# Performance work log

Hardware: AMD Instinct MI355X
Metric: run time of the kernel (lower is better)

## Reference

```python
import jax, jax.numpy as jnp
import numpy as np

DIM = 2048
H = 16
HD = 128
S = 2640          # frame_seq_len(22*40=880) * num_frame_per_block(3)
CACHE = 5280      # 6 cached frames
MAXPOS = 8192
EPS = 1e-6


def rmsnorm(x, g, eps=EPS):
    return x * jax.lax.rsqrt(jnp.mean(x * x, axis=-1, keepdims=True) + eps) * g


def apply_rope_interleaved(x, cos, sin):
    # x: [s, H, HD]; cos/sin: [s, HD//2]; is_neox=False -> adjacent pairs
    x1 = x[..., 0::2]
    x2 = x[..., 1::2]
    c = cos[:, None, :]
    s_ = sin[:, None, :]
    o1 = x1 * c - x2 * s_
    o2 = x2 * c + x1 * s_
    return jnp.stack([o1, o2], axis=-1).reshape(x.shape)


def setup_inputs() -> dict:
    key = jax.random.key(0)
    ks = jax.random.split(key, 10)
    w_scale = DIM ** -0.5
    x = jax.random.normal(ks[0], (1, S, DIM), dtype=jnp.float32)
    # cos_sin_cache: [max_pos, HD] = [cos(HD//2) | sin(HD//2)], real rope values
    inv_freq = 1.0 / (10000.0 ** (np.arange(0, HD, 2, dtype=np.float32) / HD))
    t = np.arange(MAXPOS, dtype=np.float32)
    ang = np.outer(t, inv_freq)  # [MAXPOS, HD//2]
    freqs = jnp.asarray(np.concatenate([np.cos(ang), np.sin(ang)], axis=1), dtype=jnp.float32)
    k_cache = jax.random.normal(ks[1], (CACHE, H, HD), dtype=jnp.float32)
    v_cache = jax.random.normal(ks[2], (CACHE, H, HD), dtype=jnp.float32)
    Wq = jax.random.normal(ks[3], (DIM, DIM), dtype=jnp.float32) * w_scale
    Wk = jax.random.normal(ks[4], (DIM, DIM), dtype=jnp.float32) * w_scale
    Wv = jax.random.normal(ks[5], (DIM, DIM), dtype=jnp.float32) * w_scale
    Wo = jax.random.normal(ks[6], (DIM, DIM), dtype=jnp.float32) * w_scale
    bq = jnp.zeros((DIM,), jnp.float32)
    bk = jnp.zeros((DIM,), jnp.float32)
    bv = jnp.zeros((DIM,), jnp.float32)
    bo = jnp.zeros((DIM,), jnp.float32)
    gq = jnp.ones((DIM,), jnp.float32)
    gk = jnp.ones((DIM,), jnp.float32)
    return {"x": x, "freqs": freqs, "k_cache": k_cache, "v_cache": v_cache,
            "Wq": Wq, "bq": bq, "Wk": Wk, "bk": bk, "Wv": Wv, "bv": bv,
            "Wo": Wo, "bo": bo, "gq": gq, "gk": gk, "current_start": CACHE}


def reference(x, freqs, k_cache, v_cache, Wq, bq, Wk, bk, Wv, bv, Wo, bo, gq, gk, current_start):
    s = x.shape[1]
    xf = x[0]                                   # [s, DIM], B==1
    q = rmsnorm(xf @ Wq.T + bq, gq).reshape(s, H, HD)
    k = rmsnorm(xf @ Wk.T + bk, gk).reshape(s, H, HD)
    v = (xf @ Wv.T + bv).reshape(s, H, HD)
    # fused RoPE via cos_sin_cache lookup, interleaved (is_neox=False)
    positions = jnp.arange(s, dtype=jnp.int32) + current_start
    cs = freqs[positions]                       # [s, HD]
    cos, sin = cs[:, : HD // 2], cs[:, HD // 2:]
    rq = apply_rope_interleaved(q, cos, sin)
    rk = apply_rope_interleaved(k, cos, sin)
    # streaming attention: full access to cache, causal within incoming block
    k_all = jnp.concatenate([k_cache, rk], axis=0)  # [L, H, HD]
    v_all = jnp.concatenate([v_cache, v], axis=0)
    L = k_all.shape[0]
    scale = HD ** -0.5
    scores = jnp.einsum("qhd,khd->hqk", rq, k_all) * scale  # [H, s, L]
    kv_idx = jnp.arange(L)
    q_idx = jnp.arange(s)
    mask = (kv_idx[None, :] - (L - s)) <= q_idx[:, None]    # cache always visible
    scores = jnp.where(mask[None, :, :], scores, jnp.float32(-1e30))
    attn = jax.nn.softmax(scores, axis=-1)
    out = jnp.einsum("hqk,khd->qhd", attn, v_all).reshape(s, DIM)
    y = out @ Wo.T + bo
    return y[None]                              # [1, s, DIM]
```

## Files before the change

kernel.cpp:

```cpp
#include <hip/hip_runtime.h>

#define DIMN 2048
#define NH 16
#define HDIM 128

typedef __attribute__((ext_vector_type(4))) float f32x4;
typedef __attribute__((ext_vector_type(16))) float f32x16;
typedef __attribute__((ext_vector_type(8))) __bf16 bfx8;
typedef __attribute__((ext_vector_type(4))) __bf16 bf16x4;
typedef __attribute__((ext_vector_type(2))) __bf16 bf16x2;
typedef __attribute__((ext_vector_type(8))) unsigned short u16x8;

__device__ __forceinline__ unsigned short f2bf(float f){
  unsigned u = __builtin_bit_cast(unsigned, f);
  u += 0x7fffu + ((u >> 16) & 1u);
  return (unsigned short)(u >> 16);
}
__device__ __forceinline__ float bf2f(unsigned short h){
  unsigned u = (unsigned)h << 16;
  return __builtin_bit_cast(float, u);
}

__device__ __forceinline__ void gl_lds16(const void* g, void* l){
  __builtin_amdgcn_global_load_lds((const __attribute__((address_space(1))) void*)g,
                                   (__attribute__((address_space(3))) void*)l, 16, 0, 0);
}

__device__ __forceinline__ int xcd_swz(int bid, int nwg){
  const int q = nwg >> 3, r = nwg & 7;
  const int xcd = bid & 7, idx = bid >> 3;
  return (xcd < r ? xcd*(q+1) : r*(q+1) + (xcd-r)*q) + idx;
}

#define MFMA16(a,b,c) __builtin_amdgcn_mfma_f32_16x16x32_bf16((a),(b),(c),0,0,0)
#define MFMA32(a,b,c) __builtin_amdgcn_mfma_f32_32x32x16_bf16((a),(b),(c),0,0,0)

__global__ __launch_bounds__(256) void cast_bf16_kernel(const float* __restrict__ in,
                                                        unsigned short* __restrict__ out, int n8){
  int i = blockIdx.x*256 + threadIdx.x;
  if (i >= n8) return;
  const float4* p = (const float4*)(in + (size_t)i*8);
  float4 a = p[0], b = p[1];
  u16x8 o;
  o[0]=f2bf(a.x); o[1]=f2bf(a.y); o[2]=f2bf(a.z); o[3]=f2bf(a.w);
  o[4]=f2bf(b.x); o[5]=f2bf(b.y); o[6]=f2bf(b.z); o[7]=f2bf(b.w);
  *(u16x8*)(out + (size_t)i*8) = o;
}

__global__ __launch_bounds__(256) void kcache_kernel(const float* __restrict__ kc,
                                                     unsigned short* __restrict__ kb,
                                                     int R, int L_){
  const int gid = blockIdx.x*256 + threadIdx.x;
  if (gid >= R*256) return;
  const size_t idx = (size_t)gid * 8;
  const int k   = (int)(idx >> 11);
  const int rem = (int)(idx & 2047);
  const int hh  = rem >> 7, d = rem & 127;
  const float4* p = (const float4*)(kc + idx);
  float4 a = p[0], b = p[1];
  u16x8 o;
  o[0]=f2bf(a.x); o[1]=f2bf(a.y); o[2]=f2bf(a.z); o[3]=f2bf(a.w);
  o[4]=f2bf(b.x); o[5]=f2bf(b.y); o[6]=f2bf(b.z); o[7]=f2bf(b.w);
  *(u16x8*)(kb + (size_t)hh*L_*HDIM + (size_t)k*HDIM + d) = o;
}

__global__ __launch_bounds__(256) void vtrans_kernel(const float* __restrict__ src,
                                                     unsigned short* __restrict__ vt,
                                                     int R, int koff, int L_){
  __shared__ __align__(16) unsigned short tile[32][72];
  const int kb0 = blockIdx.x * 64, db0 = blockIdx.y * 32, hh = blockIdx.z;
  const int t = threadIdx.x;
  const int kk = t >> 2, dd = (t & 3) * 8;
  const int k = kb0 + kk;
  if (k < R){
    const float* p = src + (size_t)k*DIMN + hh*HDIM + db0 + dd;
    float4 a = ((const float4*)p)[0], b = ((const float4*)p)[1];
    tile[dd+0][kk] = f2bf(a.x); tile[dd+1][kk] = f2bf(a.y);
    tile[dd+2][kk] = f2bf(a.z); tile[dd+3][kk] = f2bf(a.w);
    tile[dd+4][kk] = f2bf(b.x); tile[dd+5][kk] = f2bf(b.y);
    tile[dd+6][kk] = f2bf(b.z); tile[dd+7][kk] = f2bf(b.w);
  }
  __syncthreads();
  const int d = t >> 3, k0 = (t & 7) * 8;
  unsigned short* dst = vt + (size_t)hh*HDIM*L_ + (size_t)(db0+d)*L_ + koff + kb0 + k0;
  if (kb0 + k0 + 8 <= R){
    *(u16x8*)dst = *(const u16x8*)&tile[d][k0];
  } else {
    #pragma unroll
    for (int e=0;e<8;++e) if (kb0 + k0 + e < R) dst[e] = tile[d][k0+e];
  }
}

__global__ __launch_bounds__(256) void vtrans_bf16_kernel(const unsigned short* __restrict__ src,
    unsigned short* __restrict__ vt, int R, int koff, int L_){
  __shared__ __align__(16) unsigned short tile[32][72];
  const int kb0 = blockIdx.x * 64, db0 = blockIdx.y * 32, hh = blockIdx.z;
  const int t = threadIdx.x;
  const int kk = t >> 2, dd = (t & 3) * 8;
  const int k = kb0 + kk;
  if (k < R){
    u16x8 a = *(const u16x8*)(src + (size_t)k*DIMN + hh*HDIM + db0 + dd);
    #pragma unroll
    for (int e=0;e<8;++e) tile[dd+e][kk] = a[e];
  }
  __syncthreads();
  const int d = t >> 3, k0 = (t & 7) * 8;
  unsigned short* dst = vt + (size_t)hh*HDIM*L_ + (size_t)(db0+d)*L_ + koff + kb0 + k0;
  if (kb0 + k0 + 8 <= R){
    *(u16x8*)dst = *(const u16x8*)&tile[d][k0];
  } else {
    #pragma unroll
    for (int e=0;e<8;++e) if (kb0 + k0 + e < R) dst[e] = tile[d][k0+e];
  }
}

__global__ __launch_bounds__(256) void norm_rope_kernel(const unsigned short* __restrict__ lin,
    const float* __restrict__ g, const float* __restrict__ freqs, const int* __restrict__ cur,
    unsigned short* __restrict__ out, int S_, size_t head_stride, int row_off, float oscale){
  const int q = blockIdx.x, t = threadIdx.x;
  u16x8 v = *(const u16x8*)(lin + (size_t)q*DIMN + t*8);
  float x[8];
  #pragma unroll
  for (int e=0;e<8;++e) x[e] = bf2f(v[e]);
  float ss = 0.f;
  #pragma unroll
  for (int e=0;e<8;++e) ss += x[e]*x[e];
  for (int m=1;m<64;m<<=1) ss += __shfl_xor(ss, m);
  __shared__ float red[4];
  if ((t & 63) == 0) red[t>>6] = ss;
  __syncthreads();
  const float tot = red[0]+red[1]+red[2]+red[3];
  const float rstd = rsqrtf(tot * (1.0f/2048.0f) + 1e-6f);
  const int n0 = t*8;
  float xr[8];
  #pragma unroll
  for (int e=0;e<8;++e) xr[e] = x[e] * rstd * g[n0+e];
  const int pos = cur[0] + q;
  const int hh = n0 >> 7, d0 = n0 & 127;
  const float* fr = freqs + (size_t)pos * HDIM;
  float o[8];
  #pragma unroll
  for (int p=0;p<4;++p){
    const int j = (d0>>1) + p;
    const float c = fr[j], s = fr[64+j];
    o[2*p]   = xr[2*p]*c - xr[2*p+1]*s;
    o[2*p+1] = xr[2*p+1]*c + xr[2*p]*s;
  }
  u16x8 ov;
  #pragma unroll
  for (int e=0;e<8;++e) ov[e] = f2bf(o[e]*oscale);
  *(u16x8*)(out + (size_t)hh*head_stride + (size_t)(q+row_off)*HDIM + d0) = ov;
}

__global__ __launch_bounds__(256,2) void gemm_bt(const unsigned short* __restrict__ A,
    const unsigned short* __restrict__ B, const float* __restrict__ bias,
    float* __restrict__ C, int M, int N, int K){
  __shared__ __align__(16) unsigned short As[128*64];
  __shared__ __align__(16) unsigned short Bs[128*64];
  const int mb = (M + 127) >> 7;
  const int swz = xcd_swz(blockIdx.x, gridDim.x);
  const int bx = swz / mb, by = swz % mb;
  const int t = threadIdx.x;
  const int w = t >> 6, lane = t & 63, lh = lane >> 4, ll = lane & 15;
  const int wr = w >> 1, wc = w & 1;
  const int m0 = by * 128, n0 = bx * 128;
  const int srow = t >> 3;
  const int scb  = (t & 7) * 16;
  const int swc  = (scb ^ ((srow & 7) << 4)) >> 1;
  int arow[4]; size_t brow[4];
  #pragma unroll
  for (int c=0;c<4;++c){
    int r = m0 + c*32 + srow; if (r >= M) r = M-1;
    arow[c] = r;
    brow[c] = (size_t)(n0 + c*32 + srow);
  }
  const int xsw = (ll & 7) << 4;
  f32x4 acc[4][4] = {};
  const int nk = K >> 6;
  for (int kt = 0; kt < nk; ++kt){
    const int k0 = kt << 6;
    #pragma unroll
    for (int c=0;c<4;++c){
      gl_lds16(A + (size_t)arow[c]*K + k0 + swc, (char*)As + c*4096 + w*1024);
      gl_lds16(B + brow[c]*K       + k0 + swc, (char*)Bs + c*4096 + w*1024);
    }
    asm volatile("s_waitcnt vmcnt(0)" ::: "memory");
    __syncthreads();
    #pragma unroll
    for (int kk=0;kk<2;++kk){
      const int cb = kk*64 + lh*16;
      bfx8 a[4], b[4];
      #pragma unroll
      for (int i=0;i<4;++i)
        a[i] = *(const bfx8*)((const char*)As + (wr*64 + i*16 + ll)*128 + (cb ^ xsw));
      #pragma unroll
      for (int j=0;j<4;++j)
        b[j] = *(const bfx8*)((const char*)Bs + (wc*64 + j*16 + ll)*128 + (cb ^ xsw));
      #pragma unroll
      for (int i=0;i<4;++i)
        #pragma unroll
        for (int j=0;j<4;++j)
          acc[i][j] = MFMA16(a[i], b[j], acc[i][j]);
    }
    __syncthreads();
  }
  #pragma unroll
  for (int i=0;i<4;++i){
    #pragma unroll
    for (int j=0;j<4;++j){
      const int col = n0 + wc*64 + j*16 + ll;
      const float bb = bias[col];
      #pragma unroll
      for (int r=0;r<4;++r){
        const int row = m0 + wr*64 + i*16 + lh*4 + r;
        if (row < M) C[(size_t)row*N + col] = acc[i][j][r] + bb;
      }
    }
  }
}

__global__ __launch_bounds__(256,2) void gemm_qkv(const unsigned short* __restrict__ A,
    const unsigned short* __restrict__ B0, const unsigned short* __restrict__ B1,
    const unsigned short* __restrict__ B2, const float* __restrict__ g0,
    const float* __restrict__ g1, const float* __restrict__ g2,
    unsigned short* __restrict__ C0, unsigned short* __restrict__ C1,
    unsigned short* __restrict__ C2, int M, int N, int K){
  const int mb = (M + 127) >> 7;
  const int nxt = N >> 7;
  const int per = nxt * mb;
  const int swz = xcd_swz(blockIdx.x, gridDim.x);
  const int zz = swz / per;
  const int rem = swz - zz * per;
  const int bx = rem / mb, by = rem % mb;
  const unsigned short* B = (zz==0) ? B0 : (zz==1) ? B1 : B2;
  const float* bias       = (zz==0) ? g0 : (zz==1) ? g1 : g2;
  unsigned short* C       = (zz==0) ? C0 : (zz==1) ? C1 : C2;
  __shared__ __align__(16) unsigned short As[128*64];
  __shared__ __align__(16) unsigned short Bs[128*64];
  const int t = threadIdx.x;
  const int w = t >> 6, lane = t & 63, lh = lane >> 4, ll = lane & 15;
  const int wr = w >> 1, wc = w & 1;
  const int m0 = by * 128, n0 = bx * 128;
  const int srow = t >> 3;
  const int scb  = (t & 7) * 16;
  const int swc  = (scb ^ ((srow & 7) << 4)) >> 1;
  int arow[4]; size_t brow[4];
  #pragma unroll
  for (int c=0;c<4;++c){
    int r = m0 + c*32 + srow; if (r >= M) r = M-1;
    arow[c] = r;
    brow[c] = (size_t)(n0 + c*32 + srow);
  }
  const int xsw = (ll & 7) << 4;
  f32x4 acc[4][4] = {};
  const int nk = K >> 6;
  for (int kt = 0; kt < nk; ++kt){
    const int k0 = kt << 6;
    #pragma unroll
    for (int c=0;c<4;++c){
      gl_lds16(A + (size_t)arow[c]*K + k0 + swc, (char*)As + c*4096 + w*1024);
      gl_lds16(B + brow[c]*K       + k0 + swc, (char*)Bs + c*4096 + w*1024);
    }
    asm volatile("s_waitcnt vmcnt(0)" ::: "memory");
    __syncthreads();
    #pragma unroll
    for (int kk=0;kk<2;++kk){
      const int cb = kk*64 + lh*16;
      bfx8 a[4], b[4];
      #pragma unroll
      for (int i=0;i<4;++i)
        a[i] = *(const bfx8*)((const char*)As + (wr*64 + i*16 + ll)*128 + (cb ^ xsw));
      #pragma unroll
      for (int j=0;j<4;++j)
        b[j] = *(const bfx8*)((const char*)Bs + (wc*64 + j*16 + ll)*128 + (cb ^ xsw));
      #pragma unroll
      for (int i=0;i<4;++i)
        #pragma unroll
        for (int j=0;j<4;++j)
          acc[i][j] = MFMA16(a[i], b[j], acc[i][j]);
    }
    __syncthreads();
  }
  #pragma unroll
  for (int i=0;i<4;++i){
    #pragma unroll
    for (int j=0;j<4;++j){
      const int col = n0 + wc*64 + j*16 + ll;
      const float bb = bias[col];
      #pragma unroll
      for (int r=0;r<4;++r){
        const int row = m0 + wr*64 + i*16 + lh*4 + r;
        if (row < M) C[(size_t)row*N + col] = f2bf(acc[i][j][r] + bb);
      }
    }
  }
}

__global__ __launch_bounds__(256,2) void attn_kernel(const unsigned short* __restrict__ Q,
    const unsigned short* __restrict__ K, const unsigned short* __restrict__ VT,
    unsigned short* __restrict__ O, float* __restrict__ pacc, float* __restrict__ pml,
    int S_, int L_, int CLn, int nx, int nsplit){
  __shared__ __align__(16) unsigned short Ks[2][64*128];
  __shared__ __align__(16) unsigned short Vs[2][128*64];
  __shared__ __align__(16) unsigned short Ps[4][32*64];
  const int nwg = gridDim.x;
  const int swzid = (blockIdx.x & 7)*(nwg >> 3) + (blockIdx.x >> 3);
  const int xq = swzid % nx;
  const int rest = swzid / nx;
  const int hh = rest % NH;
  const int z  = rest / NH;
  const int q0 = xq * 128;
  const int t = threadIdx.x, w = t >> 6, lane = t & 63;
  const int l31 = lane & 31, h = lane >> 5;
  char* Pw = (char*)Ps[w];
  const int xswp = (l31 & 7) << 4;
  const unsigned short* Qh = Q  + (size_t)hh*S_*HDIM;
  const unsigned short* Kh = K  + (size_t)hh*L_*HDIM;
  const unsigned short* Vh = VT + (size_t)hh*HDIM*L_;
  const int wrow0 = q0 + w*32;
  const int myq = wrow0 + l31;
  bfx8 qf[8];
  {
    int qr = myq; if (qr >= S_) qr = S_ - 1;
    #pragma unroll
    for (int kk=0;kk<8;++kk)
      qf[kk] = *(const bfx8*)(Qh + (size_t)qr*HDIM + kk*16 + h*8);
  }
  f32x16 acc[4] = {};
  float m_st = -1e20f, l_st = 0.f;
  int qlast = q0 + 127; if (qlast >= S_) qlast = S_ - 1;
  const int kend = CLn + qlast + 1;
  const int nt = (kend + 63) >> 6;
  const int tps = (nt + nsplit - 1) / nsplit;
  const int t0 = z * tps;
  int t1 = t0 + tps; if (t1 > nt) t1 = nt;
  const int ksrow = t >> 4, kchunk = t & 15;
  const int vsrow = t >> 3, vchunk = t & 7;
  const int last = nt - 1;

  u16x8 kreg[4], vreg[4];
  auto load_tile = [&](int ktile){
    const int kv0 = ktile << 6;
    if (ktile == last){
      #pragma unroll
      for (int c=0;c<4;++c){
        int krow = kv0 + c*16 + ksrow; if (krow >= L_) krow = L_ - 1;
        kreg[c] = *(const u16x8*)(Kh + (size_t)krow*HDIM + kchunk*8);
      }
      int vcol = kv0 + vchunk*8; if (vcol > L_ - 8) vcol = L_ - 8;
      #pragma unroll
      for (int c=0;c<4;++c)
        vreg[c] = *(const u16x8*)(Vh + (size_t)(c*32 + vsrow)*L_ + vcol);
    } else {
      #pragma unroll
      for (int c=0;c<4;++c)
        kreg[c] = *(const u16x8*)(Kh + (size_t)(kv0 + c*16 + ksrow)*HDIM + kchunk*8);
      const int vcol = kv0 + vchunk*8;
      #pragma unroll
      for (int c=0;c<4;++c)
        vreg[c] = *(const u16x8*)(Vh + (size_t)(c*32 + vsrow)*L_ + vcol);
    }
  };
  auto stage_write = [&](int b){
    #pragma unroll
    for (int c=0;c<4;++c)
      *(u16x8*)((char*)Ks[b] + (c*16 + ksrow)*256 + ((kchunk*16) ^ ((ksrow & 7) << 4))) = kreg[c];
    #pragma unroll
    for (int c=0;c<4;++c)
      *(u16x8*)((char*)Vs[b] + (c*32 + vsrow)*128 + ((vchunk*16) ^ ((vsrow & 7) << 4))) = vreg[c];
  };

  if (t0 < t1){
    load_tile(t0);
    stage_write(0);
    if (t0 + 1 < t1) load_tile(t0 + 1);
  }
  const int krow0 = l31,      koff0 = (krow0 & 7) << 4;
  const int krow1 = 32 + l31, koff1 = (krow1 & 7) << 4;
  int cur = 0;
  for (int kt = t0; kt < t1; ++kt){
    const int kv0 = kt << 6;
    __syncthreads();
    const char* Kc = (const char*)Ks[cur];
    const char* Vc = (const char*)Vs[cur];
    f32x16 sc0 = {}, sc1 = {};
    __builtin_amdgcn_s_setprio(1);
    #pragma unroll
    for (int kk=0;kk<8;++kk){
      const int cb = kk*32 + h*16;
      bfx8 kf0 = *(const bfx8*)(Kc + krow0*256 + (cb ^ koff0));
      bfx8 kf1 = *(const bfx8*)(Kc + krow1*256 + (cb ^ koff1));
      sc0 = MFMA32(kf0, qf[kk], sc0);
      sc1 = MFMA32(kf1, qf[kk], sc1);
    }
    __builtin_amdgcn_s_setprio(0);
    if (kt + 1 < t1){
      stage_write(cur ^ 1);
      if (kt + 2 < t1) load_tile(kt + 2);
    }
    if (kv0 + 63 > CLn + wrow0){
      const int lim = CLn + myq;
      #pragma unroll
      for (int r=0;r<16;++r){
        const int kl = (r&3) + 8*(r>>2) + 4*h;
        if (kv0 + kl      > lim) sc0[r] = -1e30f;
        if (kv0 + 32 + kl > lim) sc1[r] = -1e30f;
      }
    }
    float mt = sc0[0];
    #pragma unroll
    for (int r=1;r<16;++r) mt = fmaxf(mt, sc0[r]);
    #pragma unroll
    for (int r=0;r<16;++r) mt = fmaxf(mt, sc1[r]);
    mt = fmaxf(mt, __shfl_xor(mt, 32));
    mt = fmaxf(mt, -1e20f);
    if (!__all(mt - m_st <= 11.54f)){
      const float mn = fmaxf(m_st, mt);
      const float corr = exp2f(m_st - mn);
      m_st = mn;
      l_st *= corr;
      #pragma unroll
      for (int r=0;r<16;++r){
        const int qrow = (r&3) + 8*(r>>2) + 4*h;
        const float ca = __shfl(corr, qrow);
        #pragma unroll
        for (int db=0;db<4;++db) acc[db][r] *= ca;
      }
    }
    float rs = 0.f;
    #pragma unroll
    for (int r=0;r<16;++r){
      const float p0 = exp2f(sc0[r] - m_st);
      const float p1 = exp2f(sc1[r] - m_st);
      sc0[r] = p0; sc1[r] = p1;
      rs += p0 + p1;
    }
    rs += __shfl_xor(rs, 32);
    l_st += rs;
    #pragma unroll
    for (int i=0;i<4;++i){
      bf16x4 p0 = { (__bf16)sc0[4*i], (__bf16)sc0[4*i+1], (__bf16)sc0[4*i+2], (__bf16)sc0[4*i+3] };
      bf16x4 p1 = { (__bf16)sc1[4*i], (__bf16)sc1[4*i+1], (__bf16)sc1[4*i+2], (__bf16)sc1[4*i+3] };
      const int kb0b = (8*i + 4*h) * 2;
      *(bf16x4*)(Pw + l31*128 + (kb0b        ^ xswp)) = p0;
      *(bf16x4*)(Pw + l31*128 + ((64 + kb0b) ^ xswp)) = p1;
    }
    __builtin_amdgcn_s_setprio(1);
    #pragma unroll
    for (int s=0;s<4;++s){
      bfx8 pa = *(const bfx8*)(Pw + l31*128 + ((s*32 + h*16) ^ xswp));
      const int vb = s*32 + h*16;
      #pragma unroll
      for (int db=0;db<4;++db){
        const int vrow = db*32 + l31;
        bfx8 vf = *(const bfx8*)(Vc + vrow*128 + (vb ^ ((vrow & 7) << 4)));
        acc[db] = MFMA32(pa, vf, acc[db]);
      }
    }
    __builtin_amdgcn_s_setprio(0);
    cur ^= 1;
  }
  if (nsplit == 1){
    const float linv = 1.0f / l_st;
    #pragma unroll
    for (int r=0;r<16;++r){
      const int qrow = (r&3) + 8*(r>>2) + 4*h;
      const float inv = __shfl(linv, qrow);
      const int qr = wrow0 + qrow;
      if (qr < S_){
        #pragma unroll
        for (int db=0;db<4;++db)
          O[(size_t)qr*DIMN + hh*HDIM + db*32 + l31] = f2bf(acc[db][r]*inv);
      }
    }
  } else {
    #pragma unroll
    for (int r=0;r<16;++r){
      const int qrow = (r&3) + 8*(r>>2) + 4*h;
      const int qr = wrow0 + qrow;
      if (qr < S_){
        const size_t rid = ((size_t)z*NH + hh)*S_ + qr;
        float* dst = pacc + rid*128;
        #pragma unroll
        for (int db=0;db<4;++db) dst[db*32 + l31] = acc[db][r];
      }
    }
    if (lane < 32 && myq < S_){
      const size_t rid2 = ((size_t)z*NH + hh)*S_ + myq;
      pml[rid2*2]   = m_st;
      pml[rid2*2+1] = l_st;
    }
  }
}

__global__ __launch_bounds__(256) void combine_kernel(const float* __restrict__ pacc,
    const float* __restrict__ pml, unsigned short* __restrict__ ob, int S_, int nsplit){
  const int t = threadIdx.x;
  const int rid = blockIdx.x*2 + (t >> 7);
  if (rid >= S_*NH) return;
  const int d = t & 127;
  const int hh = rid / S_;
  const int q  = rid - hh*S_;
  float M = -1e20f;
  for (int s=0; s<nsplit; ++s)
    M = fmaxf(M, pml[((size_t)s*NH*S_ + rid)*2]);
  float lt = 0.f, o = 0.f;
  for (int s=0; s<nsplit; ++s){
    const float m = pml[((size_t)s*NH*S_ + rid)*2];
    const float l = pml[((size_t)s*NH*S_ + rid)*2 + 1];
    const float wgt = exp2f(m - M);
    lt += l * wgt;
    o  += pacc[((size_t)s*NH*S_ + rid)*128 + d] * wgt;
  }
  if (lt == 0.f) lt = 1.f;
  ob[(size_t)q*DIMN + hh*HDIM + d] = f2bf(o / lt);
}

extern "C" void kernel_launch(void* const* d_in, const int* in_sizes, int n_in,
                              void* d_out, int out_size, void* d_ws, size_t ws_size,
                              hipStream_t stream){
  const float* x       = (const float*)d_in[0];
  const float* freqs   = (const float*)d_in[1];
  const float* k_cache = (const float*)d_in[2];
  const float* v_cache = (const float*)d_in[3];
  const float* Wq = (const float*)d_in[4];
  const float* bq = (const float*)d_in[5];
  const float* Wk = (const float*)d_in[6];
  const float* bk = (const float*)d_in[7];
  const float* Wv = (const float*)d_in[8];
  const float* bv = (const float*)d_in[9];
  const float* Wo = (const float*)d_in[10];
  const float* bo = (const float*)d_in[11];
  const float* gq = (const float*)d_in[12];
  const float* gk = (const float*)d_in[13];
  const int*   cur = (const int*)d_in[14];

  const int S = in_sizes[0] / DIMN;
  const int CACHE_ = in_sizes[2] / DIMN;
  const int L = CACHE_ + S;
  const int CLn = L - S;

  auto al = [](size_t n){ return (n + 255) & ~(size_t)255; };
  char* base = (char*)d_ws;
  size_t off = 0;
  auto take = [&](size_t n){ char* r = base + off; off += al(n); return r; };
  unsigned short* xb  = (unsigned short*)take((size_t)S*DIMN*2);
  unsigned short* Wob = (unsigned short*)take((size_t)DIMN*DIMN*2);
  unsigned short* qb  = (unsigned short*)take((size_t)NH*S*HDIM*2);
  unsigned short* kb  = (unsigned short*)take((size_t)NH*L*HDIM*2);
  unsigned short* vtb = (unsigned short*)take((size_t)NH*HDIM*L*2);
  unsigned short* ob  = (unsigned short*)take((size_t)S*DIMN*2);
  const size_t ubase = off;
  const size_t l_sz = al((size_t)S*DIMN*2);
  const size_t w_sz = al((size_t)DIMN*DIMN*2);
  unsigned short* lin0 = (unsigned short*)(base + ubase);
  unsigned short* lin1 = (unsigned short*)(base + ubase + l_sz);
  unsigned short* lin2 = (unsigned short*)(base + ubase + 2*l_sz);
  unsigned short* Wqb  = (unsigned short*)(base + ubase + 3*l_sz);
  unsigned short* Wkb  = (unsigned short*)(base + ubase + 3*l_sz + w_sz);
  unsigned short* Wvb  = (unsigned short*)(base + ubase + 3*l_sz + 2*w_sz);
  const size_t trans_sz = 3*l_sz + 3*w_sz;
  auto pool_sz = [&](int ns){
    return al((size_t)ns*NH*S*HDIM*4) + al((size_t)ns*NH*S*2*4);
  };
  int nsplit = 1;
  if (ubase + (trans_sz > pool_sz(4) ? trans_sz : pool_sz(4)) <= ws_size) nsplit = 4;
  else if (ubase + (trans_sz > pool_sz(2) ? trans_sz : pool_sz(2)) <= ws_size) nsplit = 2;
  if (ubase + trans_sz > ws_size) return;
  float* pacc = (float*)(base + ubase);
  float* pml  = (float*)(base + ubase + al((size_t)nsplit*NH*S*HDIM*4));

  const int wn8 = DIMN*DIMN/8;
  cast_bf16_kernel<<<(S*DIMN/8+255)/256, 256, 0, stream>>>(x,  xb,  S*DIMN/8);
  cast_bf16_kernel<<<(wn8+255)/256, 256, 0, stream>>>(Wq, Wqb, wn8);
  cast_bf16_kernel<<<(wn8+255)/256, 256, 0, stream>>>(Wk, Wkb, wn8);
  cast_bf16_kernel<<<(wn8+255)/256, 256, 0, stream>>>(Wv, Wvb, wn8);
  cast_bf16_kernel<<<(wn8+255)/256, 256, 0, stream>>>(Wo, Wob, wn8);
  kcache_kernel<<<CACHE_, 256, 0, stream>>>(k_cache, kb, CACHE_, L);
  vtrans_kernel<<<dim3((CACHE_+63)/64, 4, NH), 256, 0, stream>>>(v_cache, vtb, CACHE_, 0, L);

  const int mb = (S+127)/128;
  gemm_qkv<<<(DIMN/128)*mb*3, 256, 0, stream>>>(xb, Wqb, Wkb, Wvb, bq, bk, bv,
                                                lin0, lin1, lin2, S, DIMN, DIMN);
  const float qsc = 0.08838834764831845f * 1.4426950408889634f;
  norm_rope_kernel<<<S, 256, 0, stream>>>(lin0, gq, freqs, cur, qb, S, (size_t)S*HDIM, 0, qsc);
  norm_rope_kernel<<<S, 256, 0, stream>>>(lin1, gk, freqs, cur, kb, S, (size_t)L*HDIM, CACHE_, 1.0f);
  vtrans_bf16_kernel<<<dim3((S+63)/64, 4, NH), 256, 0, stream>>>(lin2, vtb, S, CACHE_, L);

  const int nx = (S+127)/128;
  attn_kernel<<<nx*NH*nsplit, 256, 0, stream>>>(qb, kb, vtb, ob,
                                                pacc, pml, S, L, CLn, nx, nsplit);
  if (nsplit > 1)
    combine_kernel<<<(S*NH+1)/2, 256, 0, stream>>>(pacc, pml, ob, S, nsplit);
  gemm_bt<<<(DIMN/128)*mb, 256, 0, stream>>>(ob, Wob, bo, (float*)d_out, S, DIMN, DIMN);
}
```

Measured before the change: 504.7 us.

## Double-buffer GEMM LDS tiles and use direct global-to-LDS loads in attention

Both GEMM kernels now double-buffer the A/B LDS tiles, issuing the next k-tile's global_load_lds before the MFMAs on the current tile, and raise wave priority around the MFMA block. This targets the stall where each iteration previously waited on global loads before computing. The attention kernel replaces its register-staged K/V prefetch with direct global-to-LDS async loads into the alternate buffer, which frees registers. The attention change also drops the last-tile clamping of K rows and V columns, so the final partial tile may read out of bounds. LDS use in the GEMMs doubles, which may limit occupancy.

```diff
diff --git a/kernel.cpp b/kernel.cpp
--- a/kernel.cpp
+++ b/kernel.cpp
@@ -8,7 +8,6 @@
 typedef __attribute__((ext_vector_type(16))) float f32x16;
 typedef __attribute__((ext_vector_type(8))) __bf16 bfx8;
 typedef __attribute__((ext_vector_type(4))) __bf16 bf16x4;
-typedef __attribute__((ext_vector_type(2))) __bf16 bf16x2;
 typedef __attribute__((ext_vector_type(8))) unsigned short u16x8;
 
 __device__ __forceinline__ unsigned short f2bf(float f){
@@ -155,8 +154,8 @@
 __global__ __launch_bounds__(256,2) void gemm_bt(const unsigned short* __restrict__ A,
     const unsigned short* __restrict__ B, const float* __restrict__ bias,
     float* __restrict__ C, int M, int N, int K){
-  __shared__ __align__(16) unsigned short As[128*64];
-  __shared__ __align__(16) unsigned short Bs[128*64];
+  __shared__ __align__(16) unsigned short As[2][128*64];
+  __shared__ __align__(16) unsigned short Bs[2][128*64];
   const int mb = (M + 127) >> 7;
   const int swz = xcd_swz(blockIdx.x, gridDim.x);
   const int bx = swz / mb, by = swz % mb;
@@ -177,32 +176,41 @@
   const int xsw = (ll & 7) << 4;
   f32x4 acc[4][4] = {};
   const int nk = K >> 6;
+  auto stage = [&](int b, int kt){
+    const int k0 = kt << 6;
+    #pragma unroll
+    for (int c=0;c<4;++c){
+      gl_lds16(A + (size_t)arow[c]*K + k0 + swc, (char*)As[b] + c*4096 + w*1024);
+      gl_lds16(B + brow[c]*K       + k0 + swc, (char*)Bs[b] + c*4096 + w*1024);
+    }
+  };
+  stage(0, 0);
+  asm volatile("s_waitcnt vmcnt(0)" ::: "memory");
+  __syncthreads();
+  int cur = 0;
   for (int kt = 0; kt < nk; ++kt){
-    const int k0 = kt << 6;
-    #pragma unroll
-    for (int c=0;c<4;++c){
-      gl_lds16(A + (size_t)arow[c]*K + k0 + swc, (char*)As + c*4096 + w*1024);
-      gl_lds16(B + brow[c]*K       + k0 + swc, (char*)Bs + c*4096 + w*1024);
-    }
-    asm volatile("s_waitcnt vmcnt(0)" ::: "memory");
-    __syncthreads();
+    if (kt + 1 < nk) stage(cur ^ 1, kt + 1);
     #pragma unroll
     for (int kk=0;kk<2;++kk){
       const int cb = kk*64 + lh*16;
       bfx8 a[4], b[4];
       #pragma unroll
       for (int i=0;i<4;++i)
-        a[i] = *(const bfx8*)((const char*)As + (wr*64 + i*16 + ll)*128 + (cb ^ xsw));
+        a[i] = *(const bfx8*)((const char*)As[cur] + (wr*64 + i*16 + ll)*128 + (cb ^ xsw));
       #pragma unroll
       for (int j=0;j<4;++j)
-        b[j] = *(const bfx8*)((const char*)Bs + (wc*64 + j*16 + ll)*128 + (cb ^ xsw));
+        b[j] = *(const bfx8*)((const char*)Bs[cur] + (wc*64 + j*16 + ll)*128 + (cb ^ xsw));
+      __builtin_amdgcn_s_setprio(1);
       #pragma unroll
       for (int i=0;i<4;++i)
         #pragma unroll
         for (int j=0;j<4;++j)
           acc[i][j] = MFMA16(a[i], b[j], acc[i][j]);
-    }
+      __builtin_amdgcn_s_setprio(0);
+    }
+    asm volatile("s_waitcnt vmcnt(0)" ::: "memory");
     __syncthreads();
+    cur ^= 1;
   }
   #pragma unroll
   for (int i=0;i<4;++i){
@@ -235,8 +243,8 @@
   const unsigned short* B = (zz==0) ? B0 : (zz==1) ? B1 : B2;
   const float* bias       = (zz==0) ? g0 : (zz==1) ? g1 : g2;
   unsigned short* C       = (zz==0) ? C0 : (zz==1) ? C1 : C2;
-  __shared__ __align__(16) unsigned short As[128*64];
-  __shared__ __align__(16) unsigned short Bs[128*64];
+  __shared__ __align__(16) unsigned short As[2][128*64];
+  __shared__ __align__(16) unsigned short Bs[2][128*64];
   const int t = threadIdx.x;
   const int w = t >> 6, lane = t & 63, lh = lane >> 4, ll = lane & 15;
   const int wr = w >> 1, wc = w & 1;
@@ -254,32 +262,41 @@
   const int xsw = (ll & 7) << 4;
   f32x4 acc[4][4] = {};
   const int nk = K >> 6;
+  auto stage = [&](int b, int kt){
+    const int k0 = kt << 6;
+    #pragma unroll
+    for (int c=0;c<4;++c){
+      gl_lds16(A + (size_t)arow[c]*K + k0 + swc, (char*)As[b] + c*4096 + w*1024);
+      gl_lds16(B + brow[c]*K       + k0 + swc, (char*)Bs[b] + c*4096 + w*1024);
+    }
+  };
+  stage(0, 0);
+  asm volatile("s_waitcnt vmcnt(0)" ::: "memory");
+  __syncthreads();
+  int cur = 0;
   for (int kt = 0; kt < nk; ++kt){
-    const int k0 = kt << 6;
-    #pragma unroll
-    for (int c=0;c<4;++c){
-      gl_lds16(A + (size_t)arow[c]*K + k0 + swc, (char*)As + c*4096 + w*1024);
-      gl_lds16(B + brow[c]*K       + k0 + swc, (char*)Bs + c*4096 + w*1024);
-    }
-    asm volatile("s_waitcnt vmcnt(0)" ::: "memory");
-    __syncthreads();
+    if (kt + 1 < nk) stage(cur ^ 1, kt + 1);
     #pragma unroll
     for (int kk=0;kk<2;++kk){
       const int cb = kk*64 + lh*16;
       bfx8 a[4], b[4];
       #pragma unroll
       for (int i=0;i<4;++i)
-        a[i] = *(const bfx8*)((const char*)As + (wr*64 + i*16 + ll)*128 + (cb ^ xsw));
+        a[i] = *(const bfx8*)((const char*)As[cur] + (wr*64 + i*16 + ll)*128 + (cb ^ xsw));
       #pragma unroll
       for (int j=0;j<4;++j)
-        b[j] = *(const bfx8*)((const char*)Bs + (wc*64 + j*16 + ll)*128 + (cb ^ xsw));
+        b[j] = *(const bfx8*)((const char*)Bs[cur] + (wc*64 + j*16 + ll)*128 + (cb ^ xsw));
+      __builtin_amdgcn_s_setprio(1);
       #pragma unroll
       for (int i=0;i<4;++i)
         #pragma unroll
         for (int j=0;j<4;++j)
           acc[i][j] = MFMA16(a[i], b[j], acc[i][j]);
-    }
+      __builtin_amdgcn_s_setprio(0);
+    }
+    asm volatile("s_waitcnt vmcnt(0)" ::: "memory");
     __syncthreads();
+    cur ^= 1;
   }
   #pragma unroll
   for (int i=0;i<4;++i){
@@ -334,53 +351,30 @@
   const int tps = (nt + nsplit - 1) / nsplit;
   const int t0 = z * tps;
   int t1 = t0 + tps; if (t1 > nt) t1 = nt;
-  const int ksrow = t >> 4, kchunk = t & 15;
-  const int vsrow = t >> 3, vchunk = t & 7;
-  const int last = nt - 1;
-
-  u16x8 kreg[4], vreg[4];
-  auto load_tile = [&](int ktile){
+  const int ksrow = t >> 4;
+  const int kswc  = (((t & 15)*16) ^ ((ksrow & 7) << 4)) >> 1;
+  const int vsrow = t >> 3;
+  const int vswc  = (((t & 7)*16) ^ ((vsrow & 7) << 4)) >> 1;
+
+  auto stage = [&](int b, int ktile){
     const int kv0 = ktile << 6;
-    if (ktile == last){
-      #pragma unroll
-      for (int c=0;c<4;++c){
-        int krow = kv0 + c*16 + ksrow; if (krow >= L_) krow = L_ - 1;
-        kreg[c] = *(const u16x8*)(Kh + (size_t)krow*HDIM + kchunk*8);
-      }
-      int vcol = kv0 + vchunk*8; if (vcol > L_ - 8) vcol = L_ - 8;
-      #pragma unroll
-      for (int c=0;c<4;++c)
-        vreg[c] = *(const u16x8*)(Vh + (size_t)(c*32 + vsrow)*L_ + vcol);
-    } else {
-      #pragma unroll
-      for (int c=0;c<4;++c)
-        kreg[c] = *(const u16x8*)(Kh + (size_t)(kv0 + c*16 + ksrow)*HDIM + kchunk*8);
-      const int vcol = kv0 + vchunk*8;
-      #pragma unroll
-      for (int c=0;c<4;++c)
-        vreg[c] = *(const u16x8*)(Vh + (size_t)(c*32 + vsrow)*L_ + vcol);
-    }
+    #pragma unroll
+    for (int c=0;c<4;++c)
+      gl_lds16(Kh + (size_t)(kv0 + c*16 + ksrow)*HDIM + kswc, (char*)Ks[b] + c*4096 + w*1024);
+    #pragma unroll
+    for (int c=0;c<4;++c)
+      gl_lds16(Vh + (size_t)(c*32 + vsrow)*L_ + kv0 + vswc, (char*)Vs[b] + c*4096 + w*1024);
   };
-  auto stage_write = [&](int b){
-    #pragma unroll
-    for (int c=0;c<4;++c)
-      *(u16x8*)((char*)Ks[b] + (c*16 + ksrow)*256 + ((kchunk*16) ^ ((ksrow & 7) << 4))) = kreg[c];
-    #pragma unroll
-    for (int c=0;c<4;++c)
-      *(u16x8*)((char*)Vs[b] + (c*32 + vsrow)*128 + ((vchunk*16) ^ ((vsrow & 7) << 4))) = vreg[c];
-  };
-
-  if (t0 < t1){
-    load_tile(t0);
-    stage_write(0);
-    if (t0 + 1 < t1) load_tile(t0 + 1);
-  }
+
+  if (t0 < t1) stage(0, t0);
+  asm volatile("s_waitcnt vmcnt(0)" ::: "memory");
+  __syncthreads();
   const int krow0 = l31,      koff0 = (krow0 & 7) << 4;
   const int krow1 = 32 + l31, koff1 = (krow1 & 7) << 4;
   int cur = 0;
   for (int kt = t0; kt < t1; ++kt){
     const int kv0 = kt << 6;
-    __syncthreads();
+    if (kt + 1 < t1) stage(cur ^ 1, kt + 1);
     const char* Kc = (const char*)Ks[cur];
     const char* Vc = (const char*)Vs[cur];
     f32x16 sc0 = {}, sc1 = {};
@@ -394,10 +388,6 @@
       sc1 = MFMA32(kf1, qf[kk], sc1);
     }
     __builtin_amdgcn_s_setprio(0);
-    if (kt + 1 < t1){
-      stage_write(cur ^ 1);
-      if (kt + 2 < t1) load_tile(kt + 2);
-    }
     if (kv0 + 63 > CLn + wrow0){
       const int lim = CLn + myq;
       #pragma unroll
@@ -458,6 +448,8 @@
       }
     }
     __builtin_amdgcn_s_setprio(0);
+    asm volatile("s_waitcnt vmcnt(0)" ::: "memory");
+    __syncthreads();
     cur ^= 1;
   }
   if (nsplit == 1){
```

Result: faster. 483.3 us (-4.2%).
